# Performance work log

Measured on AMD Instinct MI355X. Metric: run time of the kernel, lower is better.

The kernel has to match this reference:

```python
import jax, jax.numpy as jnp
import numpy as np

N, E, D = 100_000, 1_250_000, 64
EPS = 1e-8

def setup_inputs() -> dict:
    key = jax.random.key(0)
    ks = jax.random.split(key, 8)
    h = jax.random.normal(ks[0], (N, D), jnp.float32)
    eig = jax.random.normal(ks[1], (E, 1), jnp.float32)          # per-edge vector field
    snorm_n = jax.random.uniform(ks[2], (N, 1), jnp.float32)     # node norm
    src = jax.random.randint(ks[3], (E,), 0, N)
    dst = jax.random.randint(ks[4], (E,), 0, N)
    # pretrans: Linear(2D -> D); posttrans: Linear((3+1)*D -> D); torch Linear weight is [out, in]
    W1 = jax.random.normal(ks[5], (D, 2 * D), jnp.float32) / np.sqrt(2.0 * D)
    b1 = jnp.zeros((D,), jnp.float32)
    W2 = jax.random.normal(ks[6], (D, 4 * D), jnp.float32) / np.sqrt(4.0 * D)
    b2 = jnp.zeros((D,), jnp.float32)
    gamma = jnp.ones((D,), jnp.float32)   # BatchNorm1d weight
    beta = jnp.zeros((D,), jnp.float32)   # BatchNorm1d bias
    return dict(h=h, eig=eig, snorm_n=snorm_n, src=src, dst=dst,
                W1=W1, b1=b1, W2=W2, b2=b2, gamma=gamma, beta=beta)

def reference(h, eig, snorm_n, src, dst, W1, b1, W2, b2, gamma, beta):
    seg = lambda x: jax.ops.segment_sum(x, dst, num_segments=N)
    # pretrans on edges: MLP(cat[h_src, h_dst])
    z2 = jnp.concatenate([h[src], h[dst]], axis=1)   # [E, 2D]
    e = z2 @ W1.T + b1                                # [E, D]
    deg = seg(jnp.ones((E, 1), e.dtype))              # [N, 1]
    # aggregator: mean
    agg_mean = seg(e) / jnp.maximum(deg, 1.0)
    # aggregator: max (empty segments -> 0)
    agg_max = jax.ops.segment_max(e, dst, num_segments=N)
    agg_max = jnp.where(deg > 0, agg_max, 0.0)
    # aggregator: directional derivative dir_dx
    absum = seg(jnp.abs(eig))                         # [N, 1] sum of |vf| per node
    w = eig / (absum[dst] + EPS)                      # [E, 1] normalized weights
    agg_dir = jnp.abs(seg(e * w) - seg(w) * h)        # [N, D]
    # posttrans on nodes
    hc = jnp.concatenate([h, agg_mean, agg_max, agg_dir], axis=1)  # [N, 4D]
    h2 = (hc @ W2.T + b2) * snorm_n
    # BatchNorm1d (training mode: batch stats, biased variance)
    mu = jnp.mean(h2, axis=0)
    var = jnp.var(h2, axis=0)
    h2 = (h2 - mu) * jax.lax.rsqrt(var + 1e-5) * gamma + beta
    h2 = jax.nn.relu(h2)
    # residual (in_dim == out_dim); dropout p=0 is identity
    return h + h2
```

## Files before the change

### kernel.cpp

```cpp
#include <hip/hip_runtime.h>
#include <math.h>

__device__ __forceinline__ float bf2f(unsigned short s) {
    return __uint_as_float(((unsigned)s) << 16);
}
__device__ __forceinline__ unsigned short f2bf(float f) {
    unsigned u = __float_as_uint(f);
    unsigned r = (u + 0x7fffu + ((u >> 16) & 1u)) >> 16;
    return (unsigned short)r;
}

__global__ __launch_bounds__(256) void edge_rank_kernel(
    const int* __restrict__ dst, int* __restrict__ cursor, int* __restrict__ rank, int E)
{
    int e = blockIdx.x * 256 + threadIdx.x;
    if (e < E) {
        rank[e] = atomicAdd(&cursor[dst[e]], 1);
    }
}

__global__ __launch_bounds__(256) void block_reduce_kernel(
    const int* __restrict__ deg, int* __restrict__ bsum, int N)
{
    __shared__ int sd[256];
    int t = threadIdx.x;
    int i = blockIdx.x * 256 + t;
    sd[t] = (i < N) ? deg[i] : 0;
    __syncthreads();
    for (int s = 128; s > 0; s >>= 1) {
        if (t < s) sd[t] += sd[t + s];
        __syncthreads();
    }
    if (t == 0) bsum[blockIdx.x] = sd[0];
}

__global__ __launch_bounds__(1024) void scan_bsums_kernel(
    const int* __restrict__ bsum, int* __restrict__ bscan, int nb)
{
    __shared__ int sd[1024];
    int t = threadIdx.x;
    int own = (t < nb) ? bsum[t] : 0;
    sd[t] = own;
    __syncthreads();
    for (int off = 1; off < 1024; off <<= 1) {
        int v = (t >= off) ? sd[t - off] : 0;
        __syncthreads();
        sd[t] += v;
        __syncthreads();
    }
    if (t < nb) bscan[t] = sd[t] - own;
}

__global__ __launch_bounds__(256) void block_scan_kernel(
    const int* __restrict__ deg, const int* __restrict__ bscan,
    int* __restrict__ offs, int N)
{
    __shared__ int sd[256];
    int t = threadIdx.x;
    int i = blockIdx.x * 256 + t;
    int myv = (i < N) ? deg[i] : 0;
    sd[t] = myv;
    __syncthreads();
    for (int off = 1; off < 256; off <<= 1) {
        int v = (t >= off) ? sd[t - off] : 0;
        __syncthreads();
        sd[t] += v;
        __syncthreads();
    }
    if (i < N) {
        offs[i] = sd[t] - myv + bscan[blockIdx.x];
    }
}

__global__ __launch_bounds__(256) void csr_scatter_kernel(
    const int* __restrict__ src, const int* __restrict__ dst, const float* __restrict__ eig,
    const int* __restrict__ rank, const int* __restrict__ offs,
    int2* __restrict__ csr, int E)
{
    int e = blockIdx.x * 256 + threadIdx.x;
    if (e < E) {
        int dn = dst[e];
        int p = offs[dn] + rank[e];
        csr[p] = make_int2(src[e], __float_as_int(eig[e]));
    }
}

__global__ __launch_bounds__(256) void uv_kernel(
    const float* __restrict__ h, const float* __restrict__ W1, const float* __restrict__ b1,
    unsigned short* __restrict__ u, unsigned short* __restrict__ v, int N)
{
    __shared__ float wT[64 * 128];
    __shared__ float hs[64 * 68];
    int t = threadIdx.x;
    for (int idx = t; idx < 64 * 128; idx += 256) {
        int j = idx >> 7, c = idx & 127;
        int d = c & 63;
        int col = (c < 64) ? j : (64 + j);
        wT[idx] = W1[d * 128 + col];
    }
    int n0 = blockIdx.x * 64;
    for (int r = 0; r < 16; ++r) {
        int idx = r * 256 + t;
        int nl = idx >> 6, j = idx & 63;
        int n = n0 + nl;
        hs[nl * 68 + j] = (n < N) ? h[(size_t)n * 64 + j] : 0.f;
    }
    __syncthreads();

    int nb = (t & 15) * 4;
    int cb = (t >> 4) * 8;
    float acc[4][8];
#pragma unroll
    for (int i = 0; i < 4; ++i)
#pragma unroll
        for (int k = 0; k < 8; ++k) acc[i][k] = 0.f;

    for (int j = 0; j < 64; ++j) {
        float wv[8];
#pragma unroll
        for (int k = 0; k < 8; ++k) wv[k] = wT[j * 128 + cb + k];
#pragma unroll
        for (int i = 0; i < 4; ++i) {
            float hv = hs[(nb + i) * 68 + j];
#pragma unroll
            for (int k = 0; k < 8; ++k) acc[i][k] = fmaf(hv, wv[k], acc[i][k]);
        }
    }

    bool isV = (cb >= 64);
    int dbase = cb & 63;
#pragma unroll
    for (int i = 0; i < 4; ++i) {
        int n = n0 + nb + i;
        if (n < N) {
            union { unsigned short s[8]; uint4 v4; } pk;
            if (!isV) {
#pragma unroll
                for (int k = 0; k < 8; ++k) pk.s[k] = f2bf(acc[i][k]);
                *(uint4*)(u + (size_t)n * 64 + dbase) = pk.v4;
            } else {
#pragma unroll
                for (int k = 0; k < 8; ++k) pk.s[k] = f2bf(acc[i][k] + b1[dbase + k]);
                *(uint4*)(v + (size_t)n * 64 + dbase) = pk.v4;
            }
        }
    }
}

__global__ __launch_bounds__(256) void w2t_kernel(
    const float* __restrict__ W2, float* __restrict__ w2t)
{
    int idx = blockIdx.x * 256 + threadIdx.x;
    if (idx < 64 * 256) {
        int d = idx >> 8, k = idx & 255;
        w2t[k * 64 + d] = W2[idx];
    }
}

__global__ __launch_bounds__(256) void agg_kernel(
    const unsigned short* __restrict__ u, const unsigned short* __restrict__ v,
    const float* __restrict__ h,
    const int* __restrict__ offs, const int* __restrict__ degi,
    const int2* __restrict__ csr,
    unsigned short* __restrict__ agg, int N)
{
    int gw = (blockIdx.x * 256 + threadIdx.x) >> 6;
    int lane = threadIdx.x & 63;
    int n = __builtin_amdgcn_readfirstlane(gw);
    if (n >= N) return;
    int beg = offs[n];
    int dn = degi[n];

    float accs = 0.f, accd = 0.f, accm = -3.402823466e38f;
    float pa = 0.f, ps = 0.f;
    for (int i0 = 0; i0 < dn; i0 += 64) {
        int cnt = min(dn - i0, 64);
        int idxv = 0; float wvv = 0.f;
        if (lane < cnt) {
            int2 rec = csr[beg + i0 + lane];
            idxv = rec.x;
            wvv = __int_as_float(rec.y);
        }
        pa += fabsf(wvv);
        ps += wvv;
        int j = 0;
        for (; j + 4 <= cnt; j += 4) {
            int s0 = __shfl(idxv, j), s1 = __shfl(idxv, j + 1);
            int s2 = __shfl(idxv, j + 2), s3 = __shfl(idxv, j + 3);
            float w0 = __shfl(wvv, j), w1 = __shfl(wvv, j + 1);
            float w2_ = __shfl(wvv, j + 2), w3 = __shfl(wvv, j + 3);
            float u0 = bf2f(u[(size_t)s0 * 64 + lane]);
            float u1 = bf2f(u[(size_t)s1 * 64 + lane]);
            float u2 = bf2f(u[(size_t)s2 * 64 + lane]);
            float u3 = bf2f(u[(size_t)s3 * 64 + lane]);
            accs += (u0 + u1) + (u2 + u3);
            accm = fmaxf(accm, fmaxf(fmaxf(u0, u1), fmaxf(u2, u3)));
            accd = fmaf(w0, u0, fmaf(w1, u1, fmaf(w2_, u2, fmaf(w3, u3, accd))));
        }
        for (; j < cnt; ++j) {
            int s0 = __shfl(idxv, j);
            float w0 = __shfl(wvv, j);
            float u0 = bf2f(u[(size_t)s0 * 64 + lane]);
            accs += u0;
            accm = fmaxf(accm, u0);
            accd = fmaf(w0, u0, accd);
        }
    }
#pragma unroll
    for (int w = 1; w < 64; w <<= 1) {
        pa += __shfl_xor(pa, w);
        ps += __shfl_xor(ps, w);
    }
    float inv_ab = 1.f / (pa + 1e-8f);
    float segw = ps * inv_ab;

    float vl = bf2f(v[(size_t)n * 64 + lane]);
    float hl = h[(size_t)n * 64 + lane];
    float fdeg = (float)dn;
    float mean = (accs + fdeg * vl) / fmaxf(fdeg, 1.f);
    float amax = (dn > 0) ? (accm + vl) : 0.f;
    float adir = fabsf(fmaf(accd, inv_ab, segw * (vl - hl)));
    size_t base = (size_t)n * 192;
    agg[base + lane]       = f2bf(mean);
    agg[base + 64 + lane]  = f2bf(amax);
    agg[base + 128 + lane] = f2bf(adir);
}

__global__ __launch_bounds__(256) void post_gemm_kernel(
    const float* __restrict__ h, const unsigned short* __restrict__ agg,
    const float* __restrict__ w2t, const float* __restrict__ b2,
    const float* __restrict__ snorm, float* __restrict__ h2,
    float* __restrict__ bn_buf, int N)
{
    __shared__ float hcS[64 * 65];
    int tid = threadIdx.x;
    int node = tid & 63;
    int q = __builtin_amdgcn_readfirstlane(tid >> 6);
    int n0 = blockIdx.x * 64;
    int n = n0 + node;
    float acc[16];
#pragma unroll
    for (int i = 0; i < 16; ++i) acc[i] = 0.f;

    for (int c = 0; c < 4; ++c) {
        if (c == 0) {
            for (int it = 0; it < 4; ++it) {
                int idx = it * 256 + tid;
                int r = idx >> 4, c4 = idx & 15;
                int nn = n0 + r;
                float4 val = make_float4(0.f, 0.f, 0.f, 0.f);
                if (nn < N) val = *(const float4*)(h + (size_t)nn * 64 + c4 * 4);
                int kk = c4 * 4;
                hcS[(kk + 0) * 65 + r] = val.x;
                hcS[(kk + 1) * 65 + r] = val.y;
                hcS[(kk + 2) * 65 + r] = val.z;
                hcS[(kk + 3) * 65 + r] = val.w;
            }
        } else {
            for (int it = 0; it < 2; ++it) {
                int idx = it * 256 + tid;
                int r = idx >> 3, j8 = idx & 7;
                int nn = n0 + r;
                uint4 val = make_uint4(0, 0, 0, 0);
                if (nn < N) val = *(const uint4*)(agg + (size_t)nn * 192 + (c - 1) * 64 + j8 * 8);
                unsigned short* ps = (unsigned short*)&val;
                int kk = j8 * 8;
#pragma unroll
                for (int m = 0; m < 8; ++m)
                    hcS[(kk + m) * 65 + r] = bf2f(ps[m]);
            }
        }
        __syncthreads();
        const float* wbase = w2t + c * 64 * 64 + q * 16;
        for (int k = 0; k < 64; ++k) {
            float hv = hcS[k * 65 + node];
            const float* wr = wbase + k * 64;
#pragma unroll
            for (int i = 0; i < 16; ++i)
                acc[i] = fmaf(wr[i], hv, acc[i]);
        }
        __syncthreads();
    }

    float sn = (n < N) ? snorm[n] : 0.f;
#pragma unroll
    for (int i = 0; i < 16; ++i) acc[i] = (acc[i] + b2[q * 16 + i]) * sn;

    if (n < N) {
#pragma unroll
        for (int i = 0; i < 4; ++i) {
            float4 o = make_float4(acc[i * 4], acc[i * 4 + 1], acc[i * 4 + 2], acc[i * 4 + 3]);
            *(float4*)(h2 + (size_t)n * 64 + q * 16 + i * 4) = o;
        }
    }

#pragma unroll
    for (int i = 0; i < 16; ++i) hcS[(q * 16 + i) * 65 + node] = acc[i];
    __syncthreads();
    if (tid < 64) {
        float s1 = 0.f, s2 = 0.f;
        for (int r = 0; r < 64; ++r) {
            float x = hcS[tid * 65 + r];
            s1 += x;
            s2 = fmaf(x, x, s2);
        }
        atomicAdd(&bn_buf[tid], s1);
        atomicAdd(&bn_buf[64 + tid], s2);
    }
}

__global__ __launch_bounds__(256) void bn_final_kernel(
    const float* __restrict__ h, const float* __restrict__ h2,
    const float* __restrict__ bn_buf, const float* __restrict__ gamma,
    const float* __restrict__ beta, float* __restrict__ out, int N, float invN)
{
    int idx = blockIdx.x * 256 + threadIdx.x;
    int total4 = N * 16;
    if (idx >= total4) return;
    int base = idx * 4;
    int d0 = base & 63;
    const float4 a = *(const float4*)(h2 + base);
    const float4 hh = *(const float4*)(h + base);
    float r[4] = {a.x, a.y, a.z, a.w};
    float hv[4] = {hh.x, hh.y, hh.z, hh.w};
    float o[4];
#pragma unroll
    for (int k = 0; k < 4; ++k) {
        int d = d0 + k;
        float mu = bn_buf[d] * invN;
        float var = bn_buf[64 + d] * invN - mu * mu;
        float rstd = rsqrtf(var + 1e-5f);
        float x = (r[k] - mu) * rstd * gamma[d] + beta[d];
        o[k] = hv[k] + fmaxf(x, 0.f);
    }
    float4 ov = {o[0], o[1], o[2], o[3]};
    *(float4*)(out + base) = ov;
}

extern "C" void kernel_launch(void* const* d_in, const int* in_sizes, int n_in,
                              void* d_out, int out_size, void* d_ws, size_t ws_size,
                              hipStream_t stream)
{
    const float* h     = (const float*)d_in[0];
    const float* eig   = (const float*)d_in[1];
    const float* snorm = (const float*)d_in[2];
    const int*   src   = (const int*)d_in[3];
    const int*   dst   = (const int*)d_in[4];
    const float* W1    = (const float*)d_in[5];
    const float* b1    = (const float*)d_in[6];
    const float* W2    = (const float*)d_in[7];
    const float* b2    = (const float*)d_in[8];
    const float* gamma = (const float*)d_in[9];
    const float* beta  = (const float*)d_in[10];
    float* out = (float*)d_out;

    const int N = in_sizes[2];
    const int E = in_sizes[1];

    char* w = (char*)d_ws;
    size_t off = 0;
    auto alloc = [&](size_t bytes) -> char* {
        char* p = w + off;
        off += (bytes + 255) & ~size_t(255);
        return p;
    };
    unsigned short* u = (unsigned short*)alloc((size_t)N * 64 * 2);
    unsigned short* v = (unsigned short*)alloc((size_t)N * 64 * 2);
    float* h2 = (float*)u;
    unsigned short* agg = (unsigned short*)alloc((size_t)N * 192 * 2);
    int2* csr = (int2*)alloc((size_t)E * 8);
    int*  rank = (int*)alloc((size_t)E * 4);
    char* zero_base = w + off;
    int*   cursor = (int*)alloc((size_t)N * 4);
    float* bn_buf = (float*)alloc(128 * 4);
    size_t zero_bytes = (size_t)((char*)(bn_buf + 128) - zero_base);
    int* offs = (int*)alloc((size_t)N * 4);
    int nb = (N + 255) / 256;
    int* bsum  = (int*)alloc((size_t)nb * 4);
    int* bscan = (int*)alloc((size_t)nb * 4);
    float* w2t = (float*)alloc(64 * 256 * 4);
    (void)ws_size; (void)n_in; (void)out_size;

    hipMemsetAsync(zero_base, 0, zero_bytes, stream);

    int egrid = (E + 255) / 256;
    edge_rank_kernel<<<egrid, 256, 0, stream>>>(dst, cursor, rank, E);
    block_reduce_kernel<<<nb, 256, 0, stream>>>(cursor, bsum, N);
    scan_bsums_kernel<<<1, 1024, 0, stream>>>(bsum, bscan, nb);
    block_scan_kernel<<<nb, 256, 0, stream>>>(cursor, bscan, offs, N);
    csr_scatter_kernel<<<egrid, 256, 0, stream>>>(src, dst, eig, rank, offs, csr, E);

    int ntiles = (N + 63) / 64;
    uv_kernel<<<ntiles, 256, 0, stream>>>(h, W1, b1, u, v, N);
    w2t_kernel<<<64, 256, 0, stream>>>(W2, w2t);

    int agrid = ((size_t)N * 64 + 255) / 256;
    agg_kernel<<<agrid, 256, 0, stream>>>(u, v, h, offs, cursor, csr, agg, N);

    post_gemm_kernel<<<(N + 63) / 64, 256, 0, stream>>>(h, agg, w2t, b2, snorm,
                                                        h2, bn_buf, N);

    int fgrid = (N * 16 + 255) / 256;
    bn_final_kernel<<<fgrid, 256, 0, stream>>>(h, h2, bn_buf, gamma, beta, out, N, 1.0f / (float)N);
}
```

Before: 385.3 us.

## Replace scalar post-transform GEMM with bf16 MFMA kernel and fused BN partials

The node post-transform GEMM moves from an LDS-staged scalar FMA loop to bf16 MFMA 16x16x32 instructions. W2 is stored as bf16 and held in registers, and a bf16 copy of h is written by the uv kernel. Each block now covers 256 nodes. BatchNorm partial sums are reduced with shuffles before the atomics, which drops the LDS transpose and the syncthreads. The cost is an extra bf16 h buffer write, lower precision for the h and W2 inputs, and fewer blocks.

```diff
diff --git a/kernel.cpp b/kernel.cpp
--- a/kernel.cpp
+++ b/kernel.cpp
@@ -9,6 +9,9 @@
     unsigned r = (u + 0x7fffu + ((u >> 16) & 1u)) >> 16;
     return (unsigned short)r;
 }
+
+typedef __attribute__((ext_vector_type(8))) short short8v;
+typedef __attribute__((ext_vector_type(4))) float f32x4;
 
 __global__ __launch_bounds__(256) void edge_rank_kernel(
     const int* __restrict__ dst, int* __restrict__ cursor, int* __restrict__ rank, int E)
@@ -87,7 +90,8 @@
 
 __global__ __launch_bounds__(256) void uv_kernel(
     const float* __restrict__ h, const float* __restrict__ W1, const float* __restrict__ b1,
-    unsigned short* __restrict__ u, unsigned short* __restrict__ v, int N)
+    unsigned short* __restrict__ u, unsigned short* __restrict__ v,
+    unsigned short* __restrict__ hb, int N)
 {
     __shared__ float wT[64 * 128];
     __shared__ float hs[64 * 68];
@@ -107,6 +111,18 @@
     }
     __syncthreads();
 
+    for (int it = 0; it < 2; ++it) {
+        int idx = it * 256 + t;
+        int nl = idx >> 3, j8 = idx & 7;
+        int n = n0 + nl;
+        if (n < N) {
+            union { unsigned short s[8]; uint4 v4; } pk;
+#pragma unroll
+            for (int m = 0; m < 8; ++m) pk.s[m] = f2bf(hs[nl * 68 + j8 * 8 + m]);
+            *(uint4*)(hb + (size_t)n * 64 + j8 * 8) = pk.v4;
+        }
+    }
+
     int nb = (t & 15) * 4;
     int cb = (t >> 4) * 8;
     float acc[4][8];
@@ -147,14 +163,11 @@
     }
 }
 
-__global__ __launch_bounds__(256) void w2t_kernel(
-    const float* __restrict__ W2, float* __restrict__ w2t)
+__global__ __launch_bounds__(256) void w2bf_kernel(
+    const float* __restrict__ W2, unsigned short* __restrict__ w2bf)
 {
     int idx = blockIdx.x * 256 + threadIdx.x;
-    if (idx < 64 * 256) {
-        int d = idx >> 8, k = idx & 255;
-        w2t[k * 64 + d] = W2[idx];
-    }
+    if (idx < 64 * 256) w2bf[idx] = f2bf(W2[idx]);
 }
 
 __global__ __launch_bounds__(256) void agg_kernel(
@@ -226,86 +239,82 @@
     agg[base + 128 + lane] = f2bf(adir);
 }
 
-__global__ __launch_bounds__(256) void post_gemm_kernel(
-    const float* __restrict__ h, const unsigned short* __restrict__ agg,
-    const float* __restrict__ w2t, const float* __restrict__ b2,
+__global__ __launch_bounds__(256) void post_mfma_kernel(
+    const unsigned short* __restrict__ hb, const unsigned short* __restrict__ agg,
+    const unsigned short* __restrict__ w2bf, const float* __restrict__ b2,
     const float* __restrict__ snorm, float* __restrict__ h2,
     float* __restrict__ bn_buf, int N)
 {
-    __shared__ float hcS[64 * 65];
-    int tid = threadIdx.x;
-    int node = tid & 63;
-    int q = __builtin_amdgcn_readfirstlane(tid >> 6);
-    int n0 = blockIdx.x * 64;
-    int n = n0 + node;
-    float acc[16];
-#pragma unroll
-    for (int i = 0; i < 16; ++i) acc[i] = 0.f;
-
-    for (int c = 0; c < 4; ++c) {
-        if (c == 0) {
-            for (int it = 0; it < 4; ++it) {
-                int idx = it * 256 + tid;
-                int r = idx >> 4, c4 = idx & 15;
-                int nn = n0 + r;
-                float4 val = make_float4(0.f, 0.f, 0.f, 0.f);
-                if (nn < N) val = *(const float4*)(h + (size_t)nn * 64 + c4 * 4);
-                int kk = c4 * 4;
-                hcS[(kk + 0) * 65 + r] = val.x;
-                hcS[(kk + 1) * 65 + r] = val.y;
-                hcS[(kk + 2) * 65 + r] = val.z;
-                hcS[(kk + 3) * 65 + r] = val.w;
-            }
+    int lane = threadIdx.x & 63;
+    int w = threadIdx.x >> 6;
+    int lr = lane & 15;
+    int lg = lane >> 4;
+
+    short8v a[8];
+    {
+        const unsigned short* ab = w2bf + ((size_t)(w * 16 + lr)) * 256 + lg * 8;
+#pragma unroll
+        for (int s = 0; s < 8; ++s)
+            a[s] = *(const short8v*)(ab + s * 32);
+    }
+    float4 b2v = *(const float4*)(b2 + w * 16 + lg * 4);
+    float b2a[4] = {b2v.x, b2v.y, b2v.z, b2v.w};
+
+    int n0 = blockIdx.x * 256;
+    float s1[4] = {0.f, 0.f, 0.f, 0.f}, s2[4] = {0.f, 0.f, 0.f, 0.f};
+
+#pragma unroll 2
+    for (int t = 0; t < 16; ++t) {
+        int node = n0 + t * 16 + lr;
+        bool ok = node < N;
+        short8v b[8];
+        if (ok) {
+            const unsigned short* hbp = hb  + (size_t)node * 64  + lg * 8;
+            const unsigned short* agp = agg + (size_t)node * 192 + lg * 8;
+            b[0] = *(const short8v*)(hbp);
+            b[1] = *(const short8v*)(hbp + 32);
+#pragma unroll
+            for (int s = 2; s < 8; ++s)
+                b[s] = *(const short8v*)(agp + (s - 2) * 32);
         } else {
-            for (int it = 0; it < 2; ++it) {
-                int idx = it * 256 + tid;
-                int r = idx >> 3, j8 = idx & 7;
-                int nn = n0 + r;
-                uint4 val = make_uint4(0, 0, 0, 0);
-                if (nn < N) val = *(const uint4*)(agg + (size_t)nn * 192 + (c - 1) * 64 + j8 * 8);
-                unsigned short* ps = (unsigned short*)&val;
-                int kk = j8 * 8;
-#pragma unroll
-                for (int m = 0; m < 8; ++m)
-                    hcS[(kk + m) * 65 + r] = bf2f(ps[m]);
-            }
-        }
-        __syncthreads();
-        const float* wbase = w2t + c * 64 * 64 + q * 16;
-        for (int k = 0; k < 64; ++k) {
-            float hv = hcS[k * 65 + node];
-            const float* wr = wbase + k * 64;
-#pragma unroll
-            for (int i = 0; i < 16; ++i)
-                acc[i] = fmaf(wr[i], hv, acc[i]);
-        }
-        __syncthreads();
-    }
-
-    float sn = (n < N) ? snorm[n] : 0.f;
-#pragma unroll
-    for (int i = 0; i < 16; ++i) acc[i] = (acc[i] + b2[q * 16 + i]) * sn;
-
-    if (n < N) {
-#pragma unroll
-        for (int i = 0; i < 4; ++i) {
-            float4 o = make_float4(acc[i * 4], acc[i * 4 + 1], acc[i * 4 + 2], acc[i * 4 + 3]);
-            *(float4*)(h2 + (size_t)n * 64 + q * 16 + i * 4) = o;
-        }
-    }
-
-#pragma unroll
-    for (int i = 0; i < 16; ++i) hcS[(q * 16 + i) * 65 + node] = acc[i];
-    __syncthreads();
-    if (tid < 64) {
-        float s1 = 0.f, s2 = 0.f;
-        for (int r = 0; r < 64; ++r) {
-            float x = hcS[tid * 65 + r];
-            s1 += x;
-            s2 = fmaf(x, x, s2);
-        }
-        atomicAdd(&bn_buf[tid], s1);
-        atomicAdd(&bn_buf[64 + tid], s2);
+#pragma unroll
+            for (int s = 0; s < 8; ++s) b[s] = (short8v)0;
+        }
+        f32x4 acc0 = {0.f, 0.f, 0.f, 0.f}, acc1 = {0.f, 0.f, 0.f, 0.f};
+#pragma unroll
+        for (int s = 0; s < 8; s += 2) {
+            acc0 = __builtin_amdgcn_mfma_f32_16x16x32_bf16(a[s],     b[s],     acc0, 0, 0, 0);
+            acc1 = __builtin_amdgcn_mfma_f32_16x16x32_bf16(a[s + 1], b[s + 1], acc1, 0, 0, 0);
+        }
+        float sn = ok ? snorm[node] : 0.f;
+        float xr[4];
+#pragma unroll
+        for (int r = 0; r < 4; ++r) {
+            xr[r] = (acc0[r] + acc1[r] + b2a[r]) * sn;
+            s1[r] += xr[r];
+            s2[r] = fmaf(xr[r], xr[r], s2[r]);
+        }
+        if (ok) {
+            *(float4*)(h2 + (size_t)node * 64 + w * 16 + lg * 4) =
+                make_float4(xr[0], xr[1], xr[2], xr[3]);
+        }
+    }
+
+#pragma unroll
+    for (int m = 1; m < 16; m <<= 1) {
+#pragma unroll
+        for (int r = 0; r < 4; ++r) {
+            s1[r] += __shfl_xor(s1[r], m);
+            s2[r] += __shfl_xor(s2[r], m);
+        }
+    }
+    if (lr == 0) {
+        int d = w * 16 + lg * 4;
+#pragma unroll
+        for (int r = 0; r < 4; ++r) {
+            atomicAdd(&bn_buf[d + r], s1[r]);
+            atomicAdd(&bn_buf[64 + d + r], s2[r]);
+        }
     }
 }
 
@@ -368,6 +377,7 @@
     unsigned short* v = (unsigned short*)alloc((size_t)N * 64 * 2);
     float* h2 = (float*)u;
     unsigned short* agg = (unsigned short*)alloc((size_t)N * 192 * 2);
+    unsigned short* hb  = (unsigned short*)alloc((size_t)N * 64 * 2);
     int2* csr = (int2*)alloc((size_t)E * 8);
     int*  rank = (int*)alloc((size_t)E * 4);
     char* zero_base = w + off;
@@ -378,7 +388,7 @@
     int nb = (N + 255) / 256;
     int* bsum  = (int*)alloc((size_t)nb * 4);
     int* bscan = (int*)alloc((size_t)nb * 4);
-    float* w2t = (float*)alloc(64 * 256 * 4);
+    unsigned short* w2bf = (unsigned short*)alloc(64 * 256 * 2);
     (void)ws_size; (void)n_in; (void)out_size;
 
     hipMemsetAsync(zero_base, 0, zero_bytes, stream);
@@ -391,14 +401,14 @@
     csr_scatter_kernel<<<egrid, 256, 0, stream>>>(src, dst, eig, rank, offs, csr, E);
 
     int ntiles = (N + 63) / 64;
-    uv_kernel<<<ntiles, 256, 0, stream>>>(h, W1, b1, u, v, N);
-    w2t_kernel<<<64, 256, 0, stream>>>(W2, w2t);
+    uv_kernel<<<ntiles, 256, 0, stream>>>(h, W1, b1, u, v, hb, N);
+    w2bf_kernel<<<64, 256, 0, stream>>>(W2, w2bf);
 
     int agrid = ((size_t)N * 64 + 255) / 256;
     agg_kernel<<<agrid, 256, 0, stream>>>(u, v, h, offs, cursor, csr, agg, N);
 
-    post_gemm_kernel<<<(N + 63) / 64, 256, 0, stream>>>(h, agg, w2t, b2, snorm,
-                                                        h2, bn_buf, N);
+    post_mfma_kernel<<<(N + 255) / 256, 256, 0, stream>>>(hb, agg, w2bf, b2, snorm,
+                                                          h2, bn_buf, N);
 
     int fgrid = (N * 16 + 255) / 256;
     bn_final_kernel<<<fgrid, 256, 0, stream>>>(h, h2, bn_buf, gamma, beta, out, N, 1.0f / (float)N);
```

Result: faster. 374.6 us (-2.8%).
